# Performance work log

Hardware: AMD Instinct MI355X
Metric: run time of the kernel (lower is better)

The kernel has to match this reference:

```python
import jax, jax.numpy as jnp
import numpy as np

N = 100000      # number of nodes / matrix dim
D = 128         # feature width of inp
DEG = 32        # average degree -> E = 2*N*DEG random edges + N self loops


def setup_inputs() -> dict:
    key = jax.random.key(0)
    k1, k2, k3, k4 = jax.random.split(key, 4)
    E = 2 * N * DEG
    diag = jnp.arange(N, dtype=jnp.int32)
    rows = jnp.concatenate([jax.random.randint(k1, (E,), 0, N, dtype=jnp.int32), diag])
    cols = jnp.concatenate([jax.random.randint(k2, (E,), 0, N, dtype=jnp.int32), diag])
    vals = jax.random.uniform(k3, (E + N,), dtype=jnp.float32)  # torch.rand(len(edges))
    inp = jax.random.normal(k4, (N, D), dtype=jnp.float32)
    bias = jnp.zeros((N,), dtype=jnp.float32)
    return {"inp": inp, "rows": rows, "cols": cols, "vals": vals, "bias": bias}


def reference(inp, rows, cols, vals, bias):
    # out = sparse.mm(W, inp) + bias  with W in COO form (rows, cols, vals)
    gathered = vals[:, None] * inp[cols]              # [nnz, D] irregular gather
    out = jax.ops.segment_sum(gathered, rows, num_segments=N)  # scatter-add by row
    return out + bias[:, None]
```

## Files before the change

### kernel.cpp

```cpp
#include <hip/hip_runtime.h>


#define N_FEAT      128
#define R_TILE      64
#define TILE_SHIFT  6
#define COL_MASK    0x1FFFF
#define TILE_CAP    2048
#define LSORT_CAP   13312
#define REC_CAP     4608
#define SORT_K      (LSORT_CAP / 512)
#define SORT_P      (SORT_K / 2)

typedef unsigned int uint32;

__device__ __forceinline__ unsigned short f2bf(float f) {
    unsigned int u = __float_as_uint(f);
    u = (u + 0x7FFFu + ((u >> 16) & 1u)) >> 16;
    return (unsigned short)u;
}

__device__ __forceinline__ uint32 pack_rec(int r, int c, float v) {
    const uint32 qv = __float2uint_rn(v * 511.0f) & 0x1FFu;
    return (qv << 23) | ((uint32)(r & (R_TILE - 1)) << 17) | (uint32)c;
}

__global__ __launch_bounds__(512)
void local_sort_kernel(const int* __restrict__ rows,
                       const int* __restrict__ cols,
                       const float* __restrict__ vals, int nnz,
                       uint32* __restrict__ records,
                       int* __restrict__ loc, int n_tiles,
                       const float* __restrict__ inp_f,
                       ushort* __restrict__ inpb, int n4) {
    __shared__ uint32 slab[LSORT_CAP];
    __shared__ int    cnt[TILE_CAP];
    __shared__ int    wsum[8];

    const int b    = blockIdx.x;
    const int e0   = b * LSORT_CAP;
    const int e1   = min(e0 + LSORT_CAP, nnz);
    const int cntE = e1 - e0;
    const int tid  = threadIdx.x;
    const int lane = tid & 63, wv = tid >> 6;

    for (int i = tid; i < TILE_CAP; i += 512) cnt[i] = 0;
    __syncthreads();

    uint32 rec[SORT_K];
    int    til[SORT_K];
#pragma unroll
    for (int k = 0; k < SORT_P; ++k) {
        const int e  = e0 + (k << 10) + (tid << 1);
        const int i0 = k << 1, i1 = i0 + 1;
        til[i0] = -1; til[i1] = -1;
        if (e + 1 < e1) {
            const int2   r2 = *reinterpret_cast<const int2*>(rows + e);
            const int2   c2 = *reinterpret_cast<const int2*>(cols + e);
            const float2 v2 = *reinterpret_cast<const float2*>(vals + e);
            rec[i0] = pack_rec(r2.x, c2.x, v2.x);
            rec[i1] = pack_rec(r2.y, c2.y, v2.y);
            til[i0] = r2.x >> TILE_SHIFT;
            til[i1] = r2.y >> TILE_SHIFT;
            atomicAdd(&cnt[til[i0]], 1);
            atomicAdd(&cnt[til[i1]], 1);
        } else if (e < e1) {
            const int   r = rows[e];
            rec[i0] = pack_rec(r, cols[e], vals[e]);
            til[i0] = r >> TILE_SHIFT;
            atomicAdd(&cnt[til[i0]], 1);
        }
    }
    __syncthreads();

    const int g  = tid << 2;
    int c0 = cnt[g + 0], c1 = cnt[g + 1], c2 = cnt[g + 2], c3 = cnt[g + 3];
    int tsum = c0 + c1 + c2 + c3;
    int v = tsum;
    for (int off = 1; off < 64; off <<= 1) {
        int u = __shfl_up(v, off);
        if (lane >= off) v += u;
    }
    if (lane == 63) wsum[wv] = v;
    __syncthreads();
    int wpre = 0;
    for (int w = 0; w < wv; ++w) wpre += wsum[w];
    const int excl = wpre + v - tsum;
    int p0 = excl, p1 = p0 + c0, p2 = p1 + c1, p3 = p2 + c2;

    const int rowbase = b * (n_tiles + 1);
    if (g + 3 <= n_tiles) {
        reinterpret_cast<int4*>(loc + rowbase)[tid] = make_int4(p0, p1, p2, p3);
    } else {
        if (g + 0 <= n_tiles) loc[rowbase + g + 0] = p0;
        if (g + 1 <= n_tiles) loc[rowbase + g + 1] = p1;
        if (g + 2 <= n_tiles) loc[rowbase + g + 2] = p2;
        if (g + 3 <= n_tiles) loc[rowbase + g + 3] = p3;
    }
    cnt[g + 0] = p0; cnt[g + 1] = p1; cnt[g + 2] = p2; cnt[g + 3] = p3;
    __syncthreads();

#pragma unroll
    for (int k = 0; k < SORT_K; ++k) {
        if (til[k] >= 0) {
            const int p = atomicAdd(&cnt[til[k]], 1);
            slab[p] = rec[k];
        }
    }
    __syncthreads();

    uint32* outp = records + (size_t)b * LSORT_CAP;
    const int nq = cntE >> 2;
    for (int i = tid; i < nq; i += 512)
        reinterpret_cast<uint4*>(outp)[i] = reinterpret_cast<uint4*>(slab)[i];
    for (int i = (nq << 2) + tid; i < cntE; i += 512)
        outp[i] = slab[i];

    for (int i = b * 512 + tid; i < n4; i += gridDim.x * 512) {
        float4 f = reinterpret_cast<const float4*>(inp_f)[i];
        ushort4 h;
        h.x = f2bf(f.x); h.y = f2bf(f.y); h.z = f2bf(f.z); h.w = f2bf(f.w);
        reinterpret_cast<ushort4*>(inpb)[i] = h;
    }
}

template <bool BF16>
__global__ __launch_bounds__(512)
void gather_kernel(const float* __restrict__ inp,
                   const ushort* __restrict__ inpb,
                   const uint32* __restrict__ records,
                   const int* __restrict__ loc,
                   int n_blocks, int n_tiles,
                   const float* __restrict__ bias,
                   float* __restrict__ out, int n_rows) {
    __shared__ uint32 raw[REC_CAP];
    __shared__ uint32 recs[REC_CAP];
    __shared__ int    rcnt[R_TILE];
    __shared__ int    rbeg[R_TILE + 1];
    __shared__ int    rcur[R_TILE];
    __shared__ int    wsum[8];
    __shared__ int    s_total;

    const int t    = blockIdx.x;
    const int tid  = threadIdx.x;
    const int lane = tid & 63, wv = tid >> 6;

    if (tid < R_TILE) rcnt[tid] = 0;

    int s0 = 0, len = 0;
    if (tid < n_blocks) {
        const int rb = tid * (n_tiles + 1);
        s0  = loc[rb + t];
        len = loc[rb + t + 1] - s0;
    }
    int v = len;
    for (int off = 1; off < 64; off <<= 1) {
        int u = __shfl_up(v, off);
        if (lane >= off) v += u;
    }
    if (lane == 63) wsum[wv] = v;
    __syncthreads();
    int wpre = 0;
    for (int w = 0; w < wv; ++w) wpre += wsum[w];
    const int myoff = wpre + v - len;
    if (tid == 511) s_total = myoff + len;
    __syncthreads();
    const int  total = s_total;
    const bool fits  = (total <= REC_CAP);

    if (fits && len > 0) {
        const uint32* src = records + (size_t)tid * LSORT_CAP + s0;
        for (int i = 0; i < len; ++i) {
            uint32 r = src[i];
            raw[myoff + i] = r;
            atomicAdd(&rcnt[(r >> 17) & (R_TILE - 1)], 1);
        }
    }
    __syncthreads();

    if (wv == 0) {
        int c = rcnt[lane];
        int s = c;
        for (int off = 1; off < 64; off <<= 1) {
            int u = __shfl_up(s, off);
            if (lane >= off) s += u;
        }
        rbeg[lane] = s - c;
        rcur[lane] = s - c;
        if (lane == 63) rbeg[R_TILE] = s;
    }
    __syncthreads();

    if (fits) {
        for (int i = tid; i < total; i += blockDim.x) {
            uint32 r = raw[i];
            int p = atomicAdd(&rcur[(r >> 17) & (R_TILE - 1)], 1);
            recs[p] = r;
        }
    }
    __syncthreads();

    const float VQ = 1.0f / 511.0f;
    const int   q  = lane >> 4;
    const int   fq = lane & 15;

#define REC_ACC(r_)                                                            \
    {                                                                          \
        float  vv_ = (float)((r_) >> 23) * VQ;                                 \
        size_t c_  = (size_t)((r_) & COL_MASK) << 7;                           \
        if (BF16) {                                                            \
            uint4 d_ = reinterpret_cast<const uint4*>(inpb + c_)[fq];          \
            a0 = fmaf(vv_, __uint_as_float(d_.x << 16),         a0);           \
            a1 = fmaf(vv_, __uint_as_float(d_.x & 0xFFFF0000u), a1);           \
            a2 = fmaf(vv_, __uint_as_float(d_.y << 16),         a2);           \
            a3 = fmaf(vv_, __uint_as_float(d_.y & 0xFFFF0000u), a3);           \
            a4 = fmaf(vv_, __uint_as_float(d_.z << 16),         a4);           \
            a5 = fmaf(vv_, __uint_as_float(d_.z & 0xFFFF0000u), a5);           \
            a6 = fmaf(vv_, __uint_as_float(d_.w << 16),         a6);           \
            a7 = fmaf(vv_, __uint_as_float(d_.w & 0xFFFF0000u), a7);           \
        } else {                                                               \
            const float4* rp_ = reinterpret_cast<const float4*>(inp + c_)      \
                              + (fq << 1);                                     \
            float4 A_ = rp_[0], B_ = rp_[1];                                   \
            a0 = fmaf(vv_, A_.x, a0); a1 = fmaf(vv_, A_.y, a1);                \
            a2 = fmaf(vv_, A_.z, a2); a3 = fmaf(vv_, A_.w, a3);                \
            a4 = fmaf(vv_, B_.x, a4); a5 = fmaf(vv_, B_.y, a5);                \
            a6 = fmaf(vv_, B_.z, a6); a7 = fmaf(vv_, B_.w, a7);                \
        }                                                                      \
    }

    for (int k = 0; k < 8; ++k) {
        const int rl  = wv * 8 + k;
        const int row = (t << TILE_SHIFT) + rl;
        if (row >= n_rows) break;

        float a0 = 0.f, a1 = 0.f, a2 = 0.f, a3 = 0.f;
        float a4 = 0.f, a5 = 0.f, a6 = 0.f, a7 = 0.f;

        if (fits) {
            const int s = rbeg[rl], e_ = rbeg[rl + 1];
            int i = s;
            for (; i + 15 < e_; i += 16) {
                { uint32 r_ = recs[i +  0 + q]; REC_ACC(r_) }
                { uint32 r_ = recs[i +  4 + q]; REC_ACC(r_) }
                { uint32 r_ = recs[i +  8 + q]; REC_ACC(r_) }
                { uint32 r_ = recs[i + 12 + q]; REC_ACC(r_) }
            }
            for (; i < e_; i += 4) {
                const int ii_ = i + q;
                if (ii_ < e_) { uint32 r_ = recs[ii_]; REC_ACC(r_) }
            }
        } else {
            for (int b2 = 0; b2 < n_blocks; ++b2) {
                const int rb2 = b2 * (n_tiles + 1);
                const int q0 = loc[rb2 + t], q1 = loc[rb2 + t + 1];
                for (int i2 = q0; i2 < q1; ++i2) {
                    uint32 r_ = records[(size_t)b2 * LSORT_CAP + i2];
                    if ((int)((r_ >> 17) & (R_TILE - 1)) == rl && q == 0) {
                        REC_ACC(r_)
                    }
                }
            }
        }

        a0 += __shfl_xor(a0, 16); a1 += __shfl_xor(a1, 16);
        a2 += __shfl_xor(a2, 16); a3 += __shfl_xor(a3, 16);
        a4 += __shfl_xor(a4, 16); a5 += __shfl_xor(a5, 16);
        a6 += __shfl_xor(a6, 16); a7 += __shfl_xor(a7, 16);
        a0 += __shfl_xor(a0, 32); a1 += __shfl_xor(a1, 32);
        a2 += __shfl_xor(a2, 32); a3 += __shfl_xor(a3, 32);
        a4 += __shfl_xor(a4, 32); a5 += __shfl_xor(a5, 32);
        a6 += __shfl_xor(a6, 32); a7 += __shfl_xor(a7, 32);

        if (q == 0) {
            const float b_ = bias[row];
            float4* op = reinterpret_cast<float4*>(out + (size_t)row * N_FEAT)
                       + (fq << 1);
            op[0] = make_float4(a0 + b_, a1 + b_, a2 + b_, a3 + b_);
            op[1] = make_float4(a4 + b_, a5 + b_, a6 + b_, a7 + b_);
        }
    }
#undef REC_ACC
}

extern "C" void kernel_launch(void* const* d_in, const int* in_sizes, int n_in,
                              void* d_out, int out_size, void* d_ws, size_t ws_size,
                              hipStream_t stream) {
    const float* inp  = (const float*)d_in[0];
    const int*   rows = (const int*)d_in[1];
    const int*   cols = (const int*)d_in[2];
    const float* vals = (const float*)d_in[3];
    const float* bias = (const float*)d_in[4];
    float*       out  = (float*)d_out;

    const int nnz      = in_sizes[1];
    const int n_rows   = in_sizes[4];
    const int n_inp    = in_sizes[0];
    const int n_tiles  = (n_rows + R_TILE - 1) / R_TILE;
    const int n_blocks = (nnz + LSORT_CAP - 1) / LSORT_CAP;

    char*   ws  = (char*)d_ws;
    size_t  off = 0;
    uint32* records = (uint32*)(ws + off);
    off += (size_t)n_blocks * LSORT_CAP * sizeof(uint32);
    int*    loc     = (int*)(ws + off);
    off += (size_t)n_blocks * (n_tiles + 1) * sizeof(int);
    off = (off + 255) & ~(size_t)255;
    ushort* inpb    = (ushort*)(ws + off);
    const bool use_bf16 = (ws_size >= off + (size_t)n_inp * sizeof(ushort));
    const int  n4 = use_bf16 ? (n_inp / 4) : 0;

    local_sort_kernel<<<n_blocks, 512, 0, stream>>>(rows, cols, vals, nnz,
                                                    records, loc, n_tiles,
                                                    inp, inpb, n4);
    if (use_bf16)
        gather_kernel<true><<<n_tiles, 512, 0, stream>>>(inp, inpb, records, loc,
                                                         n_blocks, n_tiles, bias,
                                                         out, n_rows);
    else
        gather_kernel<false><<<n_tiles, 512, 0, stream>>>(inp, inpb, records, loc,
                                                          n_blocks, n_tiles, bias,
                                                          out, n_rows);
}
```

Measured before the change: 407.6 us.

## Halve local sort chunk, re-read inputs instead of holding records in registers

Halves the per-block local sort chunk, so twice as many sort blocks run and each uses half the shared-memory slab. The kernel no longer keeps records and tile ids in registers: it reads rows once to count, then re-reads rows/cols/vals to scatter, and adds a launch-bounds occupancy hint. The tile kernel now handles up to 1024 source blocks, with each thread gathering two segments. This trades extra global reads and more segment fetches in the second kernel for higher occupancy and parallelism in the sort.

```diff
diff --git a/kernel.cpp b/kernel.cpp
--- a/kernel.cpp
+++ b/kernel.cpp
@@ -6,10 +6,9 @@
 #define TILE_SHIFT  6
 #define COL_MASK    0x1FFFF
 #define TILE_CAP    2048
-#define LSORT_CAP   13312
+#define LSORT_CAP   6656
 #define REC_CAP     4608
-#define SORT_K      (LSORT_CAP / 512)
-#define SORT_P      (SORT_K / 2)
+#define SORT_PAIRS  6
 
 typedef unsigned int uint32;
 
@@ -24,7 +23,7 @@
     return (qv << 23) | ((uint32)(r & (R_TILE - 1)) << 17) | (uint32)c;
 }
 
-__global__ __launch_bounds__(512)
+__global__ __launch_bounds__(512, 8)
 void local_sort_kernel(const int* __restrict__ rows,
                        const int* __restrict__ cols,
                        const float* __restrict__ vals, int nnz,
@@ -46,29 +45,20 @@
     for (int i = tid; i < TILE_CAP; i += 512) cnt[i] = 0;
     __syncthreads();
 
-    uint32 rec[SORT_K];
-    int    til[SORT_K];
 #pragma unroll
-    for (int k = 0; k < SORT_P; ++k) {
-        const int e  = e0 + (k << 10) + (tid << 1);
-        const int i0 = k << 1, i1 = i0 + 1;
-        til[i0] = -1; til[i1] = -1;
+    for (int k = 0; k < SORT_PAIRS; ++k) {
+        const int e = e0 + (k << 10) + (tid << 1);
         if (e + 1 < e1) {
-            const int2   r2 = *reinterpret_cast<const int2*>(rows + e);
-            const int2   c2 = *reinterpret_cast<const int2*>(cols + e);
-            const float2 v2 = *reinterpret_cast<const float2*>(vals + e);
-            rec[i0] = pack_rec(r2.x, c2.x, v2.x);
-            rec[i1] = pack_rec(r2.y, c2.y, v2.y);
-            til[i0] = r2.x >> TILE_SHIFT;
-            til[i1] = r2.y >> TILE_SHIFT;
-            atomicAdd(&cnt[til[i0]], 1);
-            atomicAdd(&cnt[til[i1]], 1);
+            const int2 r2 = *reinterpret_cast<const int2*>(rows + e);
+            atomicAdd(&cnt[r2.x >> TILE_SHIFT], 1);
+            atomicAdd(&cnt[r2.y >> TILE_SHIFT], 1);
         } else if (e < e1) {
-            const int   r = rows[e];
-            rec[i0] = pack_rec(r, cols[e], vals[e]);
-            til[i0] = r >> TILE_SHIFT;
-            atomicAdd(&cnt[til[i0]], 1);
-        }
+            atomicAdd(&cnt[rows[e] >> TILE_SHIFT], 1);
+        }
+    }
+    {
+        const int e = e0 + (SORT_PAIRS << 10) + tid;
+        if (e < e1) atomicAdd(&cnt[rows[e] >> TILE_SHIFT], 1);
     }
     __syncthreads();
 
@@ -100,10 +90,28 @@
     __syncthreads();
 
 #pragma unroll
-    for (int k = 0; k < SORT_K; ++k) {
-        if (til[k] >= 0) {
-            const int p = atomicAdd(&cnt[til[k]], 1);
-            slab[p] = rec[k];
+    for (int k = 0; k < SORT_PAIRS; ++k) {
+        const int e = e0 + (k << 10) + (tid << 1);
+        if (e + 1 < e1) {
+            const int2   r2 = *reinterpret_cast<const int2*>(rows + e);
+            const int2   c2 = *reinterpret_cast<const int2*>(cols + e);
+            const float2 v2 = *reinterpret_cast<const float2*>(vals + e);
+            const int pA = atomicAdd(&cnt[r2.x >> TILE_SHIFT], 1);
+            slab[pA] = pack_rec(r2.x, c2.x, v2.x);
+            const int pB = atomicAdd(&cnt[r2.y >> TILE_SHIFT], 1);
+            slab[pB] = pack_rec(r2.y, c2.y, v2.y);
+        } else if (e < e1) {
+            const int r = rows[e];
+            const int p = atomicAdd(&cnt[r >> TILE_SHIFT], 1);
+            slab[p] = pack_rec(r, cols[e], vals[e]);
+        }
+    }
+    {
+        const int e = e0 + (SORT_PAIRS << 10) + tid;
+        if (e < e1) {
+            const int r = rows[e];
+            const int p = atomicAdd(&cnt[r >> TILE_SHIFT], 1);
+            slab[p] = pack_rec(r, cols[e], vals[e]);
         }
     }
     __syncthreads();
@@ -146,12 +154,19 @@
 
     if (tid < R_TILE) rcnt[tid] = 0;
 
-    int s0 = 0, len = 0;
+    int s0a = 0, lena = 0, s0b = 0, lenb = 0;
     if (tid < n_blocks) {
         const int rb = tid * (n_tiles + 1);
-        s0  = loc[rb + t];
-        len = loc[rb + t + 1] - s0;
-    }
+        s0a  = loc[rb + t];
+        lena = loc[rb + t + 1] - s0a;
+    }
+    if (tid + 512 < n_blocks) {
+        const int rb = (tid + 512) * (n_tiles + 1);
+        s0b  = loc[rb + t];
+        lenb = loc[rb + t + 1] - s0b;
+    }
+    const int len = lena + lenb;
+
     int v = len;
     for (int off = 1; off < 64; off <<= 1) {
         int u = __shfl_up(v, off);
@@ -167,11 +182,19 @@
     const int  total = s_total;
     const bool fits  = (total <= REC_CAP);
 
-    if (fits && len > 0) {
-        const uint32* src = records + (size_t)tid * LSORT_CAP + s0;
-        for (int i = 0; i < len; ++i) {
+    if (fits && lena > 0) {
+        const uint32* src = records + (size_t)tid * LSORT_CAP + s0a;
+        for (int i = 0; i < lena; ++i) {
             uint32 r = src[i];
             raw[myoff + i] = r;
+            atomicAdd(&rcnt[(r >> 17) & (R_TILE - 1)], 1);
+        }
+    }
+    if (fits && lenb > 0) {
+        const uint32* src = records + (size_t)(tid + 512) * LSORT_CAP + s0b;
+        for (int i = 0; i < lenb; ++i) {
+            uint32 r = src[i];
+            raw[myoff + lena + i] = r;
             atomicAdd(&rcnt[(r >> 17) & (R_TILE - 1)], 1);
         }
     }
```

After: 422.3 us. 3.6% more time.
